# Kernel tuning notes

Measured on AMD Instinct MI355X. Metric: run time of the kernel, lower is better.

Reference implementation:

```python
import jax, jax.numpy as jnp
import numpy as np

NBATCH, NATOM, NEIGH = 16, 512, 64
NTYPE, NWAVE, NIPSIN, NORBIT = 4, 8, 3, 128
CUTOFF = 5.0
NPAIR = NATOM * NEIGH  # neighbor pairs per configuration


def _make_index_para(nipsin):
    # [0, 1,1,1, 2,...(9 times)] -> angular-order label per channel
    parts = [np.zeros(1, np.int32)]
    for i in range(1, nipsin):
        parts.append(np.full(3 ** i, i, np.int32))
    return jnp.asarray(np.concatenate(parts))


def setup_inputs() -> dict:
    key = jax.random.key(0)
    ks = jax.random.split(key, 10)
    cart = jax.random.uniform(ks[0], (NBATCH, NATOM, 3), jnp.float32) * 6.0
    numatoms = jnp.full((NBATCH,), NATOM, dtype=jnp.int32)
    species = jax.random.randint(ks[1], (NBATCH * NATOM,), 0, NTYPE).astype(jnp.int32)
    atom_index = jax.random.randint(ks[2], (2, NBATCH, NPAIR), 0, NATOM).astype(jnp.int32)
    shifts = jnp.zeros((NBATCH, NPAIR, 3), jnp.float32)  # all pairs valid (pass >-1e10 check)
    # learned parameters / buffers
    rs = jnp.tile(jnp.linspace(0.5, 4.0, NWAVE, dtype=jnp.float32)[None, :], (NTYPE, 1))
    inta = -(jax.random.uniform(ks[3], (NTYPE, NWAVE), jnp.float32) * 0.9 + 0.1)
    params = jnp.ones((NTYPE, NWAVE), jnp.float32) / float(NEIGH)
    hyper = jax.random.normal(ks[4], (1, NIPSIN, NWAVE, NORBIT), jnp.float32) * (1.0 / np.sqrt(NWAVE))
    index_para = _make_index_para(NIPSIN)
    return {"cart": cart, "numatoms": numatoms, "species": species,
            "atom_index": atom_index, "shifts": shifts,
            "rs": rs, "inta": inta, "params": params, "hyper": hyper,
            "index_para": index_para, "cutoff": CUTOFF}


def _angular(dist_vec, f_cut, nipsin):
    # dist_vec: [N,3], f_cut: [N] -> [L, N] with L = 1 + 3 + ... + 3^(nipsin-1)
    dv = dist_vec.T  # [3, N]
    orb = f_cut[None, :]
    parts = [orb]
    for _ in range(1, nipsin):
        orb = (orb[:, None, :] * dv[None, :, :]).reshape(-1, dv.shape[1])
        parts.append(orb)
    return jnp.concatenate(parts, axis=0)


def reference(cart, numatoms, species, atom_index, shifts, rs, inta, params, hyper, index_para, cutoff):
    nbatch, natom, _ = cart.shape
    totnatom = nbatch * natom
    cart_ = cart.reshape(totnatom, 3)
    # offset per-config neighbor indices to global atom ids
    offs = (jnp.arange(nbatch, dtype=atom_index.dtype) * natom)[None, :, None]
    idx12 = (atom_index + offs).reshape(2, -1)  # [2, Npairs]
    dist_vec = cart_[idx12[0]] - cart_[idx12[1]] + shifts.reshape(-1, 3)  # [Npairs,3]
    distances = jnp.linalg.norm(dist_vec, axis=-1)  # [Npairs]
    sp_j = species[idx12[1]]
    f_cut = jnp.square(0.5 * jnp.cos(distances * (jnp.pi / cutoff)) + 0.5)
    # per-pair gaussian radial basis, gathered by neighbor element type
    radial = jnp.exp(inta[sp_j] * jnp.square(distances[:, None] - rs[sp_j]))  # [Npairs, nwave]
    ang = _angular(dist_vec, f_cut, NIPSIN)  # [L, Npairs]
    orbital = ang.T[:, :, None] * radial[:, None, :]  # [Npairs, L, nwave]
    orb_coeff = params[species]  # [totnatom, nwave] (all species >= 0)
    # iteration 0 (ocmod_list is empty, so no refinement loop)
    worb = orbital * orb_coeff[idx12[1]][:, None, :]  # [Npairs, L, nwave]
    sum_worb = jax.ops.segment_sum(worb, idx12[0], num_segments=totnatom)  # [totnatom, L, nwave]
    hp = hyper[0][index_para]  # [L, nwave, norbit]
    hw = jnp.einsum('ijk,jkm->ijm', sum_worb, hp)  # [totnatom, L, norbit]
    density = jnp.sum(jnp.square(hw), axis=1)  # [totnatom, norbit]
    return density
```

## Files before the change

### kernel.cpp

```cpp
#include <hip/hip_runtime.h>

#define NBATCH  16
#define NATOM   512
#define NEIGH   64
#define NPAIR   (NATOM * NEIGH)
#define TOTPAIR (NBATCH * NPAIR)
#define TOTATOM (NBATCH * NATOM)
#define NTYPE   4
#define NWAVE   8
#define NL      13
#define NORBIT  128
#define CAP     128
#define CAPP    130
#define NSUB    8
#define SUBCAP  40
#define PAIRS_PER_SUB (NPAIR / NSUB)


__global__ __launch_bounds__(512) void fill_kernel(
    const float* __restrict__ cart,
    const int*   __restrict__ species,
    const int*   __restrict__ atom_index,
    const float* __restrict__ shifts,
    int*         __restrict__ count,
    float4*      __restrict__ bucket)
{
    const int b   = blockIdx.x >> 3;
    const int s   = blockIdx.x & 7;
    const int tid = threadIdx.x;

    __shared__ float s_cart[NATOM * 3];
    __shared__ int   s_spc [NATOM];
    __shared__ int   s_cnt [NATOM];

    s_cart[tid]        = cart[b * NATOM * 3 + tid];
    s_cart[tid + 512]  = cart[b * NATOM * 3 + tid + 512];
    s_cart[tid + 1024] = cart[b * NATOM * 3 + tid + 1024];
    s_spc[tid] = species[b * NATOM + tid];
    s_cnt[tid] = 0;
    __syncthreads();

#pragma unroll
    for (int it = 0; it < PAIRS_PER_SUB / 512; ++it) {
        int pl = s * PAIRS_PER_SUB + it * 512 + tid;
        int p  = b * NPAIR + pl;
        int il = atom_index[p];
        int jl = atom_index[TOTPAIR + p];

        float dx = s_cart[3 * il + 0] - s_cart[3 * jl + 0] + shifts[3 * p + 0];
        float dy = s_cart[3 * il + 1] - s_cart[3 * jl + 1] + shifts[3 * p + 1];
        float dz = s_cart[3 * il + 2] - s_cart[3 * jl + 2] + shifts[3 * p + 2];
        int   sp = s_spc[jl];

        int slot = atomicAdd(&s_cnt[il], 1);
        if (slot < SUBCAP) {
            bucket[((size_t)((b * NATOM + il) * NSUB + s)) * SUBCAP + slot] =
                make_float4(dx, dy, dz, __int_as_float(sp));
        }
    }
    __syncthreads();

    count[(b * NATOM + tid) * NSUB + s] = s_cnt[tid];
}

__global__ __launch_bounds__(128) void gather_kernel(
    const float* __restrict__ rs,
    const float* __restrict__ inta,
    const float* __restrict__ params,
    const float* __restrict__ cutoff_p,
    const int*   __restrict__ count,
    const float4* __restrict__ bucket,
    const float* __restrict__ hyper,
    float*       __restrict__ out)
{
    const int i   = blockIdx.x;
    const int tid = threadIdx.x;

    __shared__ float s_a [NL][CAPP];
    __shared__ float s_rp[NWAVE][CAPP];
    __shared__ float s_S [NL * NWAVE];
    __shared__ float s_tab[3 * NTYPE * NWAVE];
    __shared__ int   s_off[NSUB + 1];

    if (tid < NTYPE * NWAVE) {
        s_tab[tid]                     = rs[tid];
        s_tab[NTYPE * NWAVE + tid]     = inta[tid];
        s_tab[2 * NTYPE * NWAVE + tid] = params[tid];
    }
    if (tid == 0) {
        int o = 0;
#pragma unroll
        for (int s2 = 0; s2 < NSUB; ++s2) {
            s_off[s2] = o;
            int c = count[i * NSUB + s2];
            o += (c < SUBCAP ? c : SUBCAP);
        }
        s_off[NSUB] = o;
    }
    __syncthreads();

    int total = s_off[NSUB];
    if (total > CAP) total = CAP;

    const float pic = 3.14159265358979323846f / cutoff_p[0];

    for (int k = tid; k < total; k += 128) {
        int s2 = 0;
#pragma unroll
        for (int t = 1; t < NSUB; ++t)
            if (k >= s_off[t]) s2 = t;
        int local = k - s_off[s2];
        float4 rec = bucket[((size_t)(i * NSUB + s2)) * SUBCAP + local];

        float dx = rec.x, dy = rec.y, dz = rec.z;
        int   sp = __float_as_int(rec.w);
        float d  = sqrtf(dx * dx + dy * dy + dz * dz);

        float c  = 0.5f * __cosf(d * pic) + 0.5f;
        float fc = c * c;

        float a1 = fc * dx, a2 = fc * dy, a3 = fc * dz;
        s_a[0][k]  = fc;
        s_a[1][k]  = a1;       s_a[2][k]  = a2;       s_a[3][k]  = a3;
        s_a[4][k]  = a1 * dx;  s_a[5][k]  = a1 * dy;  s_a[6][k]  = a1 * dz;
        s_a[7][k]  = a2 * dx;  s_a[8][k]  = a2 * dy;  s_a[9][k]  = a2 * dz;
        s_a[10][k] = a3 * dx;  s_a[11][k] = a3 * dy;  s_a[12][k] = a3 * dz;

#pragma unroll
        for (int w = 0; w < NWAVE; ++w) {
            float tt = d - s_tab[sp * NWAVE + w];
            s_rp[w][k] = __expf(s_tab[NTYPE * NWAVE + sp * NWAVE + w] * tt * tt)
                       * s_tab[2 * NTYPE * NWAVE + sp * NWAVE + w];
        }
    }
    __syncthreads();

    if (tid < NL * NWAVE) {
        int l = tid >> 3, w = tid & 7;
        float S = 0.0f;
        int k = 0;
        for (; k + 1 < total; k += 2) {
            float2 av = *(const float2*)&s_a[l][k];
            float2 rv = *(const float2*)&s_rp[w][k];
            S += av.x * rv.x;
            S += av.y * rv.y;
        }
        if (k < total) S += s_a[l][k] * s_rp[w][k];
        s_S[tid] = S;
    }
    __syncthreads();

    const int m = tid;
    float acc = 0.0f;
#pragma unroll
    for (int l = 0; l < NL; ++l) {
        int ip = (l == 0) ? 0 : ((l < 4) ? 1 : 2);
        const float* hp = hyper + (size_t)ip * (NWAVE * NORBIT) + m;
        float h = 0.0f;
#pragma unroll
        for (int w = 0; w < NWAVE; ++w)
            h += s_S[l * NWAVE + w] * hp[w * NORBIT];
        acc += h * h;
    }
    out[(size_t)i * NORBIT + m] = acc;
}

extern "C" void kernel_launch(void* const* d_in, const int* in_sizes, int n_in,
                              void* d_out, int out_size, void* d_ws, size_t ws_size,
                              hipStream_t stream) {
    const float* cart       = (const float*)d_in[0];
    const int*   species    = (const int*)  d_in[2];
    const int*   atom_index = (const int*)  d_in[3];
    const float* shifts     = (const float*)d_in[4];
    const float* rs         = (const float*)d_in[5];
    const float* inta       = (const float*)d_in[6];
    const float* params     = (const float*)d_in[7];
    const float* hyper      = (const float*)d_in[8];
    const float* cutoff_p   = (const float*)d_in[10];

    int* count = (int*)d_ws;
    float4* bucket =
        (float4*)((char*)d_ws + (size_t)TOTATOM * NSUB * sizeof(int));

    float* out = (float*)d_out;

    fill_kernel<<<NBATCH * NSUB, 512, 0, stream>>>(
        cart, species, atom_index, shifts, count, bucket);

    gather_kernel<<<TOTATOM, 128, 0, stream>>>(
        rs, inta, params, cutoff_p, count, bucket, hyper, out);
}
```

Measured before the change: 109.9 us.

## Process one atom per wavefront in gather kernel and double fill subdivisions

The gather kernel now assigns one 64-lane wavefront per atom, four atoms per 256-thread block. It removes block-wide __syncthreads by using per-wave LDS regions, shuffles for the prefix offsets and readlane broadcasts of the contraction results, and keeps hyper weights in registers. The fill kernel splits each configuration into 16 sub-blocks with 32-slot buckets, which doubles its parallelism. The smaller per-sub capacity raises the risk of dropping neighbours if counts cluster, and the hand-placed s_waitcnt stands in for proper wave-level LDS synchronization.

Result: no change. 107.8 us (-1.9%).

```diff
diff --git a/kernel.cpp b/kernel.cpp
--- a/kernel.cpp
+++ b/kernel.cpp
@@ -11,10 +11,11 @@
 #define NL      13
 #define NORBIT  128
 #define CAP     128
-#define CAPP    130
-#define NSUB    8
-#define SUBCAP  40
+#define NSUB    16
+#define SUBCAP  32
 #define PAIRS_PER_SUB (NPAIR / NSUB)
+#define STR     68
+#define WLDS    1440
 
 
 __global__ __launch_bounds__(512) void fill_kernel(
@@ -25,8 +26,8 @@
     int*         __restrict__ count,
     float4*      __restrict__ bucket)
 {
-    const int b   = blockIdx.x >> 3;
-    const int s   = blockIdx.x & 7;
+    const int b   = blockIdx.x >> 4;
+    const int s   = blockIdx.x & 15;
     const int tid = threadIdx.x;
 
     __shared__ float s_cart[NATOM * 3];
@@ -63,7 +64,7 @@
     count[(b * NATOM + tid) * NSUB + s] = s_cnt[tid];
 }
 
-__global__ __launch_bounds__(128) void gather_kernel(
+__global__ __launch_bounds__(256) void gather_kernel(
     const float* __restrict__ rs,
     const float* __restrict__ inta,
     const float* __restrict__ params,
@@ -73,96 +74,129 @@
     const float* __restrict__ hyper,
     float*       __restrict__ out)
 {
-    const int i   = blockIdx.x;
-    const int tid = threadIdx.x;
-
-    __shared__ float s_a [NL][CAPP];
-    __shared__ float s_rp[NWAVE][CAPP];
-    __shared__ float s_S [NL * NWAVE];
-    __shared__ float s_tab[3 * NTYPE * NWAVE];
-    __shared__ int   s_off[NSUB + 1];
-
-    if (tid < NTYPE * NWAVE) {
-        s_tab[tid]                     = rs[tid];
-        s_tab[NTYPE * NWAVE + tid]     = inta[tid];
-        s_tab[2 * NTYPE * NWAVE + tid] = params[tid];
-    }
-    if (tid == 0) {
-        int o = 0;
-#pragma unroll
-        for (int s2 = 0; s2 < NSUB; ++s2) {
-            s_off[s2] = o;
-            int c = count[i * NSUB + s2];
-            o += (c < SUBCAP ? c : SUBCAP);
-        }
-        s_off[NSUB] = o;
-    }
-    __syncthreads();
-
-    int total = s_off[NSUB];
+    const int wid  = threadIdx.x >> 6;
+    const int lane = threadIdx.x & 63;
+    const int i    = blockIdx.x * 4 + wid;
+
+    __shared__ float smem[4 * WLDS];
+    float* aw = smem + wid * WLDS;
+
+    int c = 0;
+    if (lane < NSUB) {
+        c = count[i * NSUB + lane];
+        if (c > SUBCAP) c = SUBCAP;
+    }
+    int offs[NSUB];
+    int total = 0;
+#pragma unroll
+    for (int t = 0; t < NSUB; ++t) {
+        int v = __shfl(c, t);
+        offs[t] = total;
+        total += v;
+    }
     if (total > CAP) total = CAP;
 
     const float pic = 3.14159265358979323846f / cutoff_p[0];
 
-    for (int k = tid; k < total; k += 128) {
-        int s2 = 0;
-#pragma unroll
-        for (int t = 1; t < NSUB; ++t)
-            if (k >= s_off[t]) s2 = t;
-        int local = k - s_off[s2];
-        float4 rec = bucket[((size_t)(i * NSUB + s2)) * SUBCAP + local];
-
-        float dx = rec.x, dy = rec.y, dz = rec.z;
-        int   sp = __float_as_int(rec.w);
-        float d  = sqrtf(dx * dx + dy * dy + dz * dz);
-
-        float c  = 0.5f * __cosf(d * pic) + 0.5f;
-        float fc = c * c;
-
-        float a1 = fc * dx, a2 = fc * dy, a3 = fc * dz;
-        s_a[0][k]  = fc;
-        s_a[1][k]  = a1;       s_a[2][k]  = a2;       s_a[3][k]  = a3;
-        s_a[4][k]  = a1 * dx;  s_a[5][k]  = a1 * dy;  s_a[6][k]  = a1 * dz;
-        s_a[7][k]  = a2 * dx;  s_a[8][k]  = a2 * dy;  s_a[9][k]  = a2 * dz;
-        s_a[10][k] = a3 * dx;  s_a[11][k] = a3 * dy;  s_a[12][k] = a3 * dz;
-
+    const int l0 = lane >> 3, w0 = lane & 7;
+    const int c1 = 64 + lane;
+    const int l1 = c1 >> 3,  w1 = c1 & 7;
+    float S0 = 0.0f, S1 = 0.0f;
+
+    for (int k0 = 0; k0 < total; k0 += 64) {
+        const int chunk_n = (total - k0 < 64) ? (total - k0) : 64;
+
+        if (lane < chunk_n) {
+            int k = k0 + lane;
+            int s2 = 0;
+#pragma unroll
+            for (int t = 1; t < NSUB; ++t)
+                if (k >= offs[t]) s2 = t;
+            int local = k - offs[s2];
+            float4 rec = bucket[((size_t)(i * NSUB + s2)) * SUBCAP + local];
+
+            float dx = rec.x, dy = rec.y, dz = rec.z;
+            int   sp = __float_as_int(rec.w);
+            float d  = sqrtf(dx * dx + dy * dy + dz * dz);
+
+            float cc = 0.5f * __cosf(d * pic) + 0.5f;
+            float fc = cc * cc;
+            float a1 = fc * dx, a2 = fc * dy, a3 = fc * dz;
+
+            aw[ 0 * STR + lane] = fc;
+            aw[ 1 * STR + lane] = a1;      aw[ 2 * STR + lane] = a2;
+            aw[ 3 * STR + lane] = a3;
+            aw[ 4 * STR + lane] = a1 * dx; aw[ 5 * STR + lane] = a1 * dy;
+            aw[ 6 * STR + lane] = a1 * dz;
+            aw[ 7 * STR + lane] = a2 * dx; aw[ 8 * STR + lane] = a2 * dy;
+            aw[ 9 * STR + lane] = a2 * dz;
+            aw[10 * STR + lane] = a3 * dx; aw[11 * STR + lane] = a3 * dy;
+            aw[12 * STR + lane] = a3 * dz;
+
+#pragma unroll
+            for (int w = 0; w < NWAVE; ++w) {
+                float tt = d - rs[sp * NWAVE + w];
+                aw[(13 + w) * STR + lane] =
+                    __expf(inta[sp * NWAVE + w] * tt * tt) * params[sp * NWAVE + w];
+            }
+        }
+        asm volatile("s_waitcnt lgkmcnt(0)" ::: "memory");
+
+        {
+            const float* pa = aw + l0 * STR;
+            const float* pr = aw + (13 + w0) * STR;
+            int k2 = 0;
+            for (; k2 + 3 < chunk_n; k2 += 4) {
+                float4 av = *(const float4*)(pa + k2);
+                float4 rv = *(const float4*)(pr + k2);
+                S0 += av.x * rv.x + av.y * rv.y + av.z * rv.z + av.w * rv.w;
+            }
+            for (; k2 < chunk_n; ++k2) S0 += pa[k2] * pr[k2];
+        }
+        if (lane < NL * NWAVE - 64) {
+            const float* pa = aw + l1 * STR;
+            const float* pr = aw + (13 + w1) * STR;
+            int k2 = 0;
+            for (; k2 + 3 < chunk_n; k2 += 4) {
+                float4 av = *(const float4*)(pa + k2);
+                float4 rv = *(const float4*)(pr + k2);
+                S1 += av.x * rv.x + av.y * rv.y + av.z * rv.z + av.w * rv.w;
+            }
+            for (; k2 < chunk_n; ++k2) S1 += pa[k2] * pr[k2];
+        }
+        asm volatile("s_waitcnt lgkmcnt(0)" ::: "memory");
+    }
+
+    float h0[3][NWAVE], h1[3][NWAVE];
+#pragma unroll
+    for (int ip = 0; ip < 3; ++ip)
 #pragma unroll
         for (int w = 0; w < NWAVE; ++w) {
-            float tt = d - s_tab[sp * NWAVE + w];
-            s_rp[w][k] = __expf(s_tab[NTYPE * NWAVE + sp * NWAVE + w] * tt * tt)
-                       * s_tab[2 * NTYPE * NWAVE + sp * NWAVE + w];
-        }
-    }
-    __syncthreads();
-
-    if (tid < NL * NWAVE) {
-        int l = tid >> 3, w = tid & 7;
-        float S = 0.0f;
-        int k = 0;
-        for (; k + 1 < total; k += 2) {
-            float2 av = *(const float2*)&s_a[l][k];
-            float2 rv = *(const float2*)&s_rp[w][k];
-            S += av.x * rv.x;
-            S += av.y * rv.y;
-        }
-        if (k < total) S += s_a[l][k] * s_rp[w][k];
-        s_S[tid] = S;
-    }
-    __syncthreads();
-
-    const int m = tid;
-    float acc = 0.0f;
+            h0[ip][w] = hyper[(ip * NWAVE + w) * NORBIT + lane];
+            h1[ip][w] = hyper[(ip * NWAVE + w) * NORBIT + 64 + lane];
+        }
+
+    float acc0 = 0.0f, acc1 = 0.0f;
 #pragma unroll
     for (int l = 0; l < NL; ++l) {
-        int ip = (l == 0) ? 0 : ((l < 4) ? 1 : 2);
-        const float* hp = hyper + (size_t)ip * (NWAVE * NORBIT) + m;
-        float h = 0.0f;
-#pragma unroll
-        for (int w = 0; w < NWAVE; ++w)
-            h += s_S[l * NWAVE + w] * hp[w * NORBIT];
-        acc += h * h;
-    }
-    out[(size_t)i * NORBIT + m] = acc;
+        const int ip = (l == 0) ? 0 : ((l < 4) ? 1 : 2);
+        float hh0 = 0.0f, hh1 = 0.0f;
+#pragma unroll
+        for (int w = 0; w < NWAVE; ++w) {
+            const int ch = l * NWAVE + w;
+            float sv;
+            if (ch < 64)
+                sv = __int_as_float(__builtin_amdgcn_readlane(__float_as_int(S0), ch));
+            else
+                sv = __int_as_float(__builtin_amdgcn_readlane(__float_as_int(S1), ch - 64));
+            hh0 += sv * h0[ip][w];
+            hh1 += sv * h1[ip][w];
+        }
+        acc0 += hh0 * hh0;
+        acc1 += hh1 * hh1;
+    }
+    out[(size_t)i * NORBIT + lane]      = acc0;
+    out[(size_t)i * NORBIT + 64 + lane] = acc1;
 }
 
 extern "C" void kernel_launch(void* const* d_in, const int* in_sizes, int n_in,
@@ -187,6 +221,6 @@
     fill_kernel<<<NBATCH * NSUB, 512, 0, stream>>>(
         cart, species, atom_index, shifts, count, bucket);
 
-    gather_kernel<<<TOTATOM, 128, 0, stream>>>(
+    gather_kernel<<<TOTATOM / 4, 256, 0, stream>>>(
         rs, inta, params, cutoff_p, count, bucket, hyper, out);
 }
```
